# Optimization experiments

Hardware: AMD Instinct MI355X
Metric: run time of the kernel (lower is better)

Reference implementation:

```python
import jax, jax.numpy as jnp
import numpy as np

DIM = 192
NUM_HEADS = 6
WS = (2, 8, 8)          # (wd, wh, ww)
SHIFT = (1, 4, 4)
B, D, H, W = 2, 4, 128, 128
N_WIN_TOK = WS[0] * WS[1] * WS[2]   # 128
NW = (D // WS[0]) * (H // WS[1]) * (W // WS[2])  # 512 windows per sample


def _rel_pos_index(ws):
    d, h, w = ws
    coords = np.stack(np.meshgrid(np.arange(d), np.arange(h), np.arange(w), indexing='ij'))
    cf = coords.reshape(3, -1)
    rel = (cf[:, :, None] - cf[:, None, :]).transpose(1, 2, 0).astype(np.int64)
    rel[:, :, 0] += d - 1
    rel[:, :, 1] += h - 1
    rel[:, :, 2] += w - 1
    rel[:, :, 0] *= (2 * h - 1) * (2 * w - 1)
    rel[:, :, 1] *= 2 * w - 1
    return rel.sum(-1)  # (N, N)

REL_IDX = _rel_pos_index(WS)


def _sine_pos(HW, num_pos_feats, temperature=10000.0):
    # matches get_sine_position_encoding(normalize=True)
    scale = 2 * np.pi
    eps = 1e-6
    ones = np.ones((1, HW[0], HW[1]), np.float32)
    y = ones.cumsum(1)
    x = ones.cumsum(2)
    y = y / (y[:, -1:, :] + eps) * scale
    x = x / (x[:, :, -1:] + eps) * scale
    i = np.arange(num_pos_feats, dtype=np.float32)
    dim_t = temperature ** (2.0 * np.floor(i / 2) / num_pos_feats)
    px = x[:, :, :, None] / dim_t
    py = y[:, :, :, None] / dim_t
    px = np.stack((np.sin(px[..., 0::2]), np.cos(px[..., 1::2])), axis=4).reshape(1, HW[0], HW[1], -1)
    py = np.stack((np.sin(py[..., 0::2]), np.cos(py[..., 1::2])), axis=4).reshape(1, HW[0], HW[1], -1)
    pos = np.concatenate((py, px), axis=3)  # (1, H, W, 2*npf)
    return pos.reshape(1, HW[0] * HW[1], -1)

POS_BIAS = _sine_pos((WS[1], WS[2]), DIM // 2)  # (1, 64, DIM)


def _ln(x, w, b):
    mu = x.mean(-1, keepdims=True)
    var = x.var(-1, keepdims=True)
    return (x - mu) / jnp.sqrt(var + 1e-5) * w + b


def _qkv(x, w, b):
    B_, N, C = x.shape
    y = (x @ w.T + b).reshape(B_, N, 3, NUM_HEADS, C // NUM_HEADS).transpose(2, 0, 3, 1, 4)
    return y[0], y[1], y[2]  # each (B_, h, N, hd)


def _attn(q, k, v, mask, rpb=None):
    # q,k,v: (B_, h, N, hd); mask: (nW, N, N) or None; rpb: (h, N, N) or None
    scale = q.shape[-1] ** -0.5
    a = jnp.einsum('bhnd,bhmd->bhnm', q * scale, k)
    if rpb is not None:
        a = a + rpb[None]
    if mask is not None:
        B_, h, N, _ = a.shape
        nW = mask.shape[0]
        a = (a.reshape(B_ // nW, nW, h, N, N) + mask[None, :, None]).reshape(B_, h, N, N)
    a = jax.nn.softmax(a, axis=-1)
    out = jnp.einsum('bhnm,bhmd->bhnd', a, v)
    B_, h, N, hd = out.shape
    return out.transpose(0, 2, 1, 3).reshape(B_, N, h * hd)


def setup_inputs() -> dict:
    key = jax.random.key(0)
    ks = jax.random.split(key, 8)
    C = DIM
    hid = int(C * 2.0)
    f = lambda k, shp: jax.random.normal(k, shp, jnp.float32) * 0.02
    tbl = (2 * WS[0] - 1) * (2 * WS[1] - 1) * (2 * WS[2] - 1)
    return {
        'x': jax.random.normal(ks[0], (B, D, H, W, C), jnp.float32),
        'mask_matrix': jnp.zeros((NW, N_WIN_TOK, N_WIN_TOK), jnp.float32),
        'norm1_w': jnp.ones((C,), jnp.float32), 'norm1_b': jnp.zeros((C,), jnp.float32),
        'qkv_self_w': f(ks[1], (3 * C, C)), 'qkv_self_b': jnp.zeros((3 * C,), jnp.float32),
        'qkv_mut_w': f(ks[2], (3 * C, C)), 'qkv_mut_b': jnp.zeros((3 * C,), jnp.float32),
        'rpb_table': f(ks[3], (tbl, NUM_HEADS)),
        'proj_w': f(ks[4], (C, 2 * C)), 'proj_b': jnp.zeros((C,), jnp.float32),
        'norm2_w': jnp.ones((C,), jnp.float32), 'norm2_b': jnp.zeros((C,), jnp.float32),
        'fc11_w': f(ks[5], (hid, C)), 'fc11_b': jnp.zeros((hid,), jnp.float32),
        'fc12_w': f(ks[6], (hid, C)), 'fc12_b': jnp.zeros((hid,), jnp.float32),
        'fc2_w': f(ks[7], (C, hid)), 'fc2_b': jnp.zeros((C,), jnp.float32),
    }


def reference(x, mask_matrix, norm1_w, norm1_b, qkv_self_w, qkv_self_b,
              qkv_mut_w, qkv_mut_b, rpb_table, proj_w, proj_b,
              norm2_w, norm2_b, fc11_w, fc11_b, fc12_w, fc12_b, fc2_w, fc2_b):
    Bb, Dd, Hh, Ww_, C = x.shape
    wd, wh, ww = WS
    N = wd * wh * ww
    Nh = N // 2

    # ---- part1: windowed mutual+self attention with cyclic shift ----
    h1 = _ln(x, norm1_w, norm1_b)
    sh = jnp.roll(h1, (-SHIFT[0], -SHIFT[1], -SHIFT[2]), axis=(1, 2, 3))
    # window_partition -> (B*nW, N, C)
    xw = sh.reshape(Bb, Dd // wd, wd, Hh // wh, wh, Ww_ // ww, ww, C)
    xw = xw.transpose(0, 1, 3, 5, 2, 4, 6, 7).reshape(-1, N, C)

    # self-attention with relative position bias
    q, k, v = _qkv(xw, qkv_self_w, qkv_self_b)
    rpb = rpb_table[REL_IDX.reshape(-1)].reshape(N, N, NUM_HEADS).transpose(2, 0, 1)
    x_self = _attn(q, k, v, mask_matrix[:, :N, :N], rpb)  # (B_, N, C)

    # mutual attention (no relative bias), sine positional bias added to input
    pos = jnp.tile(jnp.asarray(POS_BIAS, x.dtype), (1, 2, 1))  # (1, N, C)
    q, k, v = _qkv(xw + pos, qkv_mut_w, qkv_mut_b)
    q1, q2 = q[:, :, :Nh], q[:, :, Nh:]
    k1, k2 = k[:, :, :Nh], k[:, :, Nh:]
    v1, v2 = v[:, :, :Nh], v[:, :, Nh:]
    m2 = mask_matrix[:, :Nh, :Nh]
    x1 = _attn(q2, k1, v1, m2)  # frame2 queries attend frame1
    x2 = _attn(q1, k2, v2, m2)
    x_out = jnp.concatenate([jnp.concatenate([x1, x2], axis=1), x_self], axis=2)  # (B_, N, 2C)
    xp = x_out @ proj_w.T + proj_b  # (B_, N, C)

    # window_reverse + roll back
    rev = xp.reshape(Bb, Dd // wd, Hh // wh, Ww_ // ww, wd, wh, ww, C)
    rev = rev.transpose(0, 1, 4, 2, 5, 3, 6, 7).reshape(Bb, Dd, Hh, Ww_, C)
    rev = jnp.roll(rev, SHIFT, axis=(1, 2, 3))
    x = x + rev

    # ---- part2: GEGLU MLP ----
    h2 = _ln(x, norm2_w, norm2_b)
    mlp = (jax.nn.gelu(h2 @ fc11_w.T + fc11_b, approximate=False) * (h2 @ fc12_w.T + fc12_b)) @ fc2_w.T + fc2_b
    return x + mlp
```

## Files before the change

kernel.cpp:

```cpp
#include <hip/hip_runtime.h>
#include <hip/hip_bf16.h>

typedef __hip_bfloat16 bf16;
typedef __attribute__((ext_vector_type(8))) short short8;
typedef __attribute__((ext_vector_type(4))) float f32x4;

#define NTOKENS 131072
#define MFMA __builtin_amdgcn_mfma_f32_16x16x32_bf16

static constexpr size_t A_OFF    = 0;
static constexpr size_t Q_OFF    = A_OFF   + (size_t)NTOKENS*192*2;
static constexpr size_t O_OFF    = Q_OFF   + (size_t)NTOKENS*576*2;
static constexpr size_t POS_OFF  = O_OFF   + (size_t)NTOKENS*384*2;
static constexpr size_t PB_OFF   = POS_OFF + (size_t)128*192*4;
static constexpr size_t RPBF_OFF = PB_OFF  + (size_t)128*576*4;
static constexpr size_t MSKF_OFF = RPBF_OFF+ (size_t)6*128*128*2;
static constexpr size_t WB_OFF   = MSKF_OFF+ (size_t)512*128*128*2;
static constexpr size_t WQS_E = 0, WQM_E = 110592, WPR_E = 221184,
                        W11_E = 294912, W12_E = 368640, W2_E = 442368, WTOT = 516096;

__device__ __forceinline__ float u2f(unsigned int ubits) {
    union { unsigned int i; float f; } c; c.i = ubits << 16; return c.f;
}
__device__ __forceinline__ unsigned pkbf(float a, float b) {
    unsigned ua = (unsigned)__bfloat16_as_ushort(__float2bfloat16(a));
    unsigned ub = (unsigned)__bfloat16_as_ushort(__float2bfloat16(b));
    return ua | (ub << 16);
}
__device__ __forceinline__ short8 u4s8(uint4 v) { union { uint4 u; short8 s; } c; c.u = v; return c.s; }

__device__ __forceinline__ void gl16(const bf16* g, void* l) {
    __builtin_amdgcn_global_load_lds(
        (const __attribute__((address_space(1))) void*)g,
        (__attribute__((address_space(3))) void*)l, 16, 0, 0);
}

__global__ __launch_bounds__(256) void cvtw_kernel(
    const float* __restrict__ a, const float* __restrict__ b, const float* __restrict__ c,
    const float* __restrict__ d, const float* __restrict__ e, const float* __restrict__ f,
    bf16* __restrict__ out) {
    int i = blockIdx.x * 256 + threadIdx.x;
    const float* src; int off;
    if      (i < (int)WQM_E) { src = a; off = (int)WQS_E; }
    else if (i < (int)WPR_E) { src = b; off = (int)WQM_E; }
    else if (i < (int)W11_E) { src = c; off = (int)WPR_E; }
    else if (i < (int)W12_E) { src = d; off = (int)W11_E; }
    else if (i < (int)W2_E)  { src = e; off = (int)W12_E; }
    else if (i < (int)WTOT)  { src = f; off = (int)W2_E; }
    else return;
    out[i] = __float2bfloat16(src[i - off]);
}

__global__ __launch_bounds__(256) void pos_kernel(float* __restrict__ pos) {
    int idx = blockIdx.x * 256 + threadIdx.x;
    if (idx >= 128 * 192) return;
    int t = idx / 192, c = idx - t * 192;
    int s = t & 63;
    int hh = s >> 3, ww = s & 7;
    const float twopi = 6.2831853071795864f;
    float coord = (c < 96) ? (float)(hh + 1) : (float)(ww + 1);
    coord = coord / (8.0f + 1e-6f) * twopi;
    int f = (c < 96) ? c : c - 96;
    float dimt = powf(10000.0f, (float)(2 * (f >> 1)) / 96.0f);
    float v = coord / dimt;
    pos[idx] = (f & 1) ? cosf(v) : sinf(v);
}

__global__ __launch_bounds__(256) void pbias_kernel(const float* __restrict__ pos,
                                                    const bf16* __restrict__ Wm,
                                                    const float* __restrict__ bqm,
                                                    float* __restrict__ PB) {
    int idx = blockIdx.x * 256 + threadIdx.x;
    if (idx >= 128 * 576) return;
    int t = idx / 576, n = idx - t * 576;
    const float* pp = pos + t * 192;
    const bf16* wp = Wm + (size_t)n * 192;
    float acc = bqm[n];
    for (int k = 0; k < 192; ++k) acc += pp[k] * __bfloat162float(wp[k]);
    PB[idx] = acc;
}

__global__ __launch_bounds__(256) void rpbF_kernel(const float* __restrict__ tbl,
                                                   bf16* __restrict__ rpbF) {
    int idx = blockIdx.x * 256 + threadIdx.x;
    if (idx >= 6 * 32 * 128 * 4) return;
    int jr = idx & 3;
    int i = (idx >> 2) & 127;
    int jq = (idx >> 9) & 31;
    int h = idx >> 14;
    int j = jq * 4 + jr;
    int di = i >> 6, hi = (i >> 3) & 7, wi = i & 7;
    int dj = j >> 6, hj = (j >> 3) & 7, wj = j & 7;
    int t = (di - dj + 1) * 225 + (hi - hj + 7) * 15 + (wi - wj + 7);
    rpbF[idx] = __float2bfloat16(tbl[t * 6 + h]);
}

__global__ __launch_bounds__(256) void mskF_kernel(const float* __restrict__ mask,
                                                   bf16* __restrict__ mskF) {
    int idx = blockIdx.x * 256 + threadIdx.x;
    int widx = idx >> 12;
    int rem = idx & 4095;
    int i = rem >> 5, jq = rem & 31;
    float4 v = *reinterpret_cast<const float4*>(mask + ((size_t)widx << 14) + i * 128 + jq * 4);
    uint2 o;
    o.x = pkbf(v.x, v.y);
    o.y = pkbf(v.z, v.w);
    *reinterpret_cast<uint2*>(mskF + ((size_t)widx << 14) + (jq * 128 + i) * 4) = o;
}

template <int PART>
__global__ __launch_bounds__(256) void ln_kernel(const float* __restrict__ xin,
                                                 const float* __restrict__ w,
                                                 const float* __restrict__ b,
                                                 bf16* __restrict__ out) {
    int tok = blockIdx.x * 4 + (threadIdx.x >> 6);
    int lane = threadIdx.x & 63;
    const float* xp = xin + (size_t)tok * 192;
    float x0 = xp[lane], x1 = xp[lane + 64], x2 = xp[lane + 128];
    float s = x0 + x1 + x2;
    float ss = x0 * x0 + x1 * x1 + x2 * x2;
    for (int off = 32; off; off >>= 1) {
        s += __shfl_xor(s, off);
        ss += __shfl_xor(ss, off);
    }
    float mean = s * (1.0f / 192.0f);
    float var = ss * (1.0f / 192.0f) - mean * mean;
    float rstd = rsqrtf(var + 1e-5f);
    size_t obase;
    if (PART) {
        int bb = tok >> 16;
        int rem = tok & 65535;
        int d = rem >> 14;
        int hw = rem & 16383;
        int hh = hw >> 7, w2 = hw & 127;
        int sd = (d + 3) & 3;
        int sh = (hh + 124) & 127;
        int sw = (w2 + 124) & 127;
        int win = ((bb * 2 + (sd >> 1)) * 16 + (sh >> 3)) * 16 + (sw >> 3);
        int t = ((sd & 1) << 6) | ((sh & 7) << 3) | (sw & 7);
        obase = ((size_t)win * 128 + t) * 192;
    } else {
        obase = (size_t)tok * 192;
    }
    out[obase + lane]       = __float2bfloat16((x0 - mean) * rstd * w[lane] + b[lane]);
    out[obase + lane + 64]  = __float2bfloat16((x1 - mean) * rstd * w[lane + 64] + b[lane + 64]);
    out[obase + lane + 128] = __float2bfloat16((x2 - mean) * rstd * w[lane + 128] + b[lane + 128]);
}

template <int MODE, int BIAS>
__global__ __launch_bounds__(256) void mgemm(
    const bf16* __restrict__ Ab, int K, int nb,
    const bf16* __restrict__ W1, const float* __restrict__ B1,
    const bf16* __restrict__ W2, const float* __restrict__ B2,
    const float* __restrict__ resid,
    void* __restrict__ outp) {
    constexpr bool DUAL = (MODE == 3);
    __shared__ __align__(16) unsigned char AsB[2][16384];

    int total = gridDim.x;
    int bid = blockIdx.x;
    int lin = (bid & 7) * (total >> 3) + (bid >> 3);
    int mb = lin / nb, nbk = lin - mb * nb;
    int m0 = mb << 7, n0 = nbk << 6;
    int tid = threadIdx.x;
    int w = tid >> 6, l = tid & 63;
    int wr = w >> 1, wc = w & 1;
    int lr = l & 15, lg = l >> 4;

    f32x4 acc[4][2] = {};
    f32x4 acc2[4][2] = {};

    auto stage = [&](int buf, int kc) {
        int k0 = kc << 6;
#pragma unroll
        for (int it = 0; it < 4; ++it) {
            int idx = it * 256 + tid;
            int row = idx >> 3, gs = idx & 7;
            int gsrc = gs ^ (row & 7);
            gl16(Ab + (size_t)(m0 + row) * K + k0 + gsrc * 8, &AsB[buf][idx * 16]);
        }
    };

    const bf16* wbase  = W1 + (size_t)(n0 + wc * 32 + lr) * K + lg * 8;
    const bf16* wbase2 = DUAL ? (W2 + (size_t)(n0 + wc * 32 + lr) * K + lg * 8) : wbase;

    uint4 wcur[2][2], wnxt[2][2];
    uint4 wcur2[2][2], wnxt2[2][2];

    int nK = K >> 6;
    stage(0, 0);
#pragma unroll
    for (int cb = 0; cb < 2; ++cb)
#pragma unroll
        for (int ks = 0; ks < 2; ++ks) {
            wcur[cb][ks] = *reinterpret_cast<const uint4*>(wbase + (size_t)cb * 16 * K + ks * 32);
            if constexpr (DUAL)
                wcur2[cb][ks] = *reinterpret_cast<const uint4*>(wbase2 + (size_t)cb * 16 * K + ks * 32);
        }
    __syncthreads();
    for (int kc = 0; kc < nK; ++kc) {
        int cur = kc & 1;
        if (kc + 1 < nK) {
            stage(cur ^ 1, kc + 1);
            int ko = (kc + 1) * 64;
#pragma unroll
            for (int cb = 0; cb < 2; ++cb)
#pragma unroll
                for (int ks = 0; ks < 2; ++ks) {
                    wnxt[cb][ks] = *reinterpret_cast<const uint4*>(
                        wbase + (size_t)cb * 16 * K + ko + ks * 32);
                    if constexpr (DUAL)
                        wnxt2[cb][ks] = *reinterpret_cast<const uint4*>(
                            wbase2 + (size_t)cb * 16 * K + ko + ks * 32);
                }
        }
        const unsigned char* as = AsB[cur];
#pragma unroll
        for (int ks = 0; ks < 2; ++ks) {
            short8 af[4];
#pragma unroll
            for (int rb = 0; rb < 4; ++rb) {
                int row = wr * 64 + rb * 16 + lr;
                af[rb] = *reinterpret_cast<const short8*>(
                    &as[(unsigned)((row * 128 + ks * 64 + lg * 16) ^ ((row & 7) << 4))]);
            }
#pragma unroll
            for (int rb = 0; rb < 4; ++rb)
#pragma unroll
                for (int cb = 0; cb < 2; ++cb) {
                    acc[rb][cb] = MFMA(af[rb], u4s8(wcur[cb][ks]), acc[rb][cb], 0, 0, 0);
                    if constexpr (DUAL)
                        acc2[rb][cb] = MFMA(af[rb], u4s8(wcur2[cb][ks]), acc2[rb][cb], 0, 0, 0);
                }
        }
        __syncthreads();
        if (kc + 1 < nK) {
#pragma unroll
            for (int cb = 0; cb < 2; ++cb)
#pragma unroll
                for (int ks = 0; ks < 2; ++ks) {
                    wcur[cb][ks] = wnxt[cb][ks];
                    if constexpr (DUAL) wcur2[cb][ks] = wnxt2[cb][ks];
                }
        }
    }

    if (MODE == 0 || MODE == 3) {
        bf16* eb = (bf16*)AsB[0];
#pragma unroll
        for (int rb = 0; rb < 4; ++rb)
#pragma unroll
            for (int r = 0; r < 4; ++r) {
                int ml = wr * 64 + rb * 16 + lg * 4 + r;
#pragma unroll
                for (int cb = 0; cb < 2; ++cb) {
                    int cl = wc * 32 + cb * 16 + lr;
                    int n = n0 + cl;
                    if (MODE == 0) {
                        float bias_v = BIAS ? resid[(ml & 127) * 576 + n] : B1[n];
                        eb[ml * 64 + cl] = __float2bfloat16(acc[rb][cb][r] + bias_v);
                    } else {
                        float u = acc[rb][cb][r] + B1[n];
                        float v2 = acc2[rb][cb][r] + B2[n];
                        float t = u * (0.7978845608028654f + 0.0356774081363001f * u * u);
                        float g = u * v2 / (1.0f + __expf(-2.0f * t));
                        eb[ml * 64 + cl] = __float2bfloat16(g);
                    }
                }
            }
        __syncthreads();
        bf16* Og = (bf16*)outp;
        const int ostr = (MODE == 0) ? 576 : 384;
#pragma unroll
        for (int it = 0; it < 4; ++it) {
            int idx = it * 256 + tid;
            int row = idx >> 3, g = idx & 7;
            uint4 v = *reinterpret_cast<const uint4*>(&eb[row * 64 + g * 8]);
            *reinterpret_cast<uint4*>(Og + (size_t)(m0 + row) * ostr + n0 + g * 8) = v;
        }
    } else {
#pragma unroll
        for (int rb = 0; rb < 4; ++rb) {
#pragma unroll
            for (int r = 0; r < 4; ++r) {
                int m = m0 + wr * 64 + rb * 16 + lg * 4 + r;
                if (MODE == 2) {
                    int win = m >> 7, t = m & 127;
                    int bb = win >> 9, rem = win & 511;
                    int sd = ((rem >> 8) << 1) | (t >> 6);
                    int sh = (((rem >> 4) & 15) << 3) | ((t >> 3) & 7);
                    int sw = ((rem & 15) << 3) | (t & 7);
                    int dq = (sd + 1) & 3;
                    int hq = (sh + 4) & 127;
                    int wq = (sw + 4) & 127;
                    size_t gb = ((((size_t)bb * 4 + dq) * 128 + hq) * 128 + wq) * 192;
                    float* Rr = (float*)outp;
#pragma unroll
                    for (int cb = 0; cb < 2; ++cb) {
                        int n = n0 + wc * 32 + cb * 16 + lr;
                        Rr[gb + n] = resid[gb + n] + acc[rb][cb][r] + B1[n];
                    }
                } else {
                    float* Og = (float*)outp;
#pragma unroll
                    for (int cb = 0; cb < 2; ++cb) {
                        int n = n0 + wc * 32 + cb * 16 + lr;
                        Og[(size_t)m * 192 + n] =
                            resid[(size_t)m * 192 + n] + acc[rb][cb][r] + B1[n];
                    }
                }
            }
        }
    }
}

__global__ __launch_bounds__(256) void attn_self(
    const bf16* __restrict__ Qb, const bf16* __restrict__ rpbF,
    const bf16* __restrict__ mskF, bf16* __restrict__ Ob) {
    __shared__ __align__(16) bf16 VtB[4096];
    __shared__ __align__(16) bf16 EpiB[4][1280];
    int bid = blockIdx.x;
    int lin = (bid & 7) * 768 + (bid >> 3);
    int widx = lin / 12, sub = lin - widx * 12;
    int h = sub % 6, b2 = sub / 6;
    int win = b2 * 512 + widx;
    int tid = threadIdx.x, w = tid >> 6, l = tid & 63;
    int lr = l & 15, lg = l >> 4;
    const float qscale = 0.17677669529663689f;
    size_t qbase = (size_t)win * 128 * 576 + h * 32;

#pragma unroll
    for (int it = 0; it < 16; ++it) {
        int idx = it * 256 + tid;
        int d = idx & 31, j = idx >> 5;
        bf16 v = Qb[qbase + (size_t)j * 576 + 384 + d];
        VtB[(d * 256 + (((j >> 3) ^ (d & 7)) << 4) + (j & 7) * 2) >> 1] = v;
    }

    uint4 kf[8], qf[2];
#pragma unroll
    for (int jb = 0; jb < 8; ++jb)
        kf[jb] = *reinterpret_cast<const uint4*>(Qb + qbase + (size_t)(jb * 16 + lr) * 576 + 192 + lg * 8);
    int i0 = w * 32;
#pragma unroll
    for (int ib = 0; ib < 2; ++ib)
        qf[ib] = *reinterpret_cast<const uint4*>(Qb + qbase + (size_t)(i0 + ib * 16 + lr) * 576 + lg * 8);
    f32x4 s[8][2] = {};
#pragma unroll
    for (int jb = 0; jb < 8; ++jb)
#pragma unroll
        for (int ib = 0; ib < 2; ++ib)
            s[jb][ib] = MFMA(u4s8(kf[jb]), u4s8(qf[ib]), s[jb][ib], 0, 0, 0);

    const bf16* rpF = rpbF + (size_t)h * 16384;
    const bf16* mpF = mskF + (size_t)widx * 16384;
#pragma unroll
    for (int jb = 0; jb < 8; ++jb) {
        int jq0 = jb * 4 + lg;
#pragma unroll
        for (int ib = 0; ib < 2; ++ib) {
            int il = i0 + ib * 16 + lr;
            uint2 rv = *reinterpret_cast<const uint2*>(rpF + (jq0 * 128 + il) * 4);
            uint2 mv = *reinterpret_cast<const uint2*>(mpF + (jq0 * 128 + il) * 4);
            s[jb][ib][0] = fmaf(s[jb][ib][0], qscale, u2f(rv.x & 0xffffu) + u2f(mv.x & 0xffffu));
            s[jb][ib][1] = fmaf(s[jb][ib][1], qscale, u2f(rv.x >> 16) + u2f(mv.x >> 16));
            s[jb][ib][2] = fmaf(s[jb][ib][2], qscale, u2f(rv.y & 0xffffu) + u2f(mv.y & 0xffffu));
            s[jb][ib][3] = fmaf(s[jb][ib][3], qscale, u2f(rv.y >> 16) + u2f(mv.y >> 16));
        }
    }

    float rs[2];
    unsigned w0[2][8], w1[2][8];
#pragma unroll
    for (int ib = 0; ib < 2; ++ib) {
        float mx = -1e30f;
#pragma unroll
        for (int jb = 0; jb < 8; ++jb)
#pragma unroll
            for (int r = 0; r < 4; ++r) mx = fmaxf(mx, s[jb][ib][r]);
        mx = fmaxf(mx, __shfl_xor(mx, 16));
        mx = fmaxf(mx, __shfl_xor(mx, 32));
        float sum = 0.0f;
#pragma unroll
        for (int jb = 0; jb < 8; ++jb)
#pragma unroll
            for (int r = 0; r < 4; ++r) {
                float e = __expf(s[jb][ib][r] - mx);
                s[jb][ib][r] = e;
                sum += e;
            }
        sum += __shfl_xor(sum, 16);
        sum += __shfl_xor(sum, 32);
        rs[ib] = 1.0f / sum;
#pragma unroll
        for (int jb = 0; jb < 8; ++jb) {
            w0[ib][jb] = pkbf(s[jb][ib][0], s[jb][ib][1]);
            w1[ib][jb] = pkbf(s[jb][ib][2], s[jb][ib][3]);
        }
    }
    __syncthreads();

    f32x4 o[2][2] = {};
    int srcA = lr + 16 * (2 * (lg & 1));
    int srcB = srcA + 16;
    bool hi = ((lg >> 1) & 1) != 0;
#pragma unroll
    for (int ks = 0; ks < 4; ++ks) {
        short8 vt[2];
#pragma unroll
        for (int db = 0; db < 2; ++db) {
            int d = db * 16 + lr;
            vt[db] = *reinterpret_cast<const short8*>(
                &VtB[(d * 256 + (((ks * 4 + lg) ^ (d & 7)) << 4)) >> 1]);
        }
#pragma unroll
        for (int ib = 0; ib < 2; ++ib) {
            unsigned xa0 = (unsigned)__shfl((int)w0[ib][2 * ks], srcA, 64);
            unsigned xa1 = (unsigned)__shfl((int)w0[ib][2 * ks + 1], srcA, 64);
            unsigned xb0 = (unsigned)__shfl((int)w1[ib][2 * ks], srcA, 64);
            unsigned xb1 = (unsigned)__shfl((int)w1[ib][2 * ks + 1], srcA, 64);
            unsigned xc0 = (unsigned)__shfl((int)w0[ib][2 * ks], srcB, 64);
            unsigned xc1 = (unsigned)__shfl((int)w0[ib][2 * ks + 1], srcB, 64);
            unsigned xd0 = (unsigned)__shfl((int)w1[ib][2 * ks], srcB, 64);
            unsigned xd1 = (unsigned)__shfl((int)w1[ib][2 * ks + 1], srcB, 64);
            uint4 bfv;
            bfv.x = hi ? xa1 : xa0;
            bfv.y = hi ? xb1 : xb0;
            bfv.z = hi ? xc1 : xc0;
            bfv.w = hi ? xd1 : xd0;
            short8 pb = u4s8(bfv);
#pragma unroll
            for (int db = 0; db < 2; ++db) o[db][ib] = MFMA(vt[db], pb, o[db][ib], 0, 0, 0);
        }
    }

    bf16* eb = &EpiB[w][0];
#pragma unroll
    for (int db = 0; db < 2; ++db)
#pragma unroll
        for (int ib = 0; ib < 2; ++ib)
#pragma unroll
            for (int r = 0; r < 4; ++r) {
                int d = db * 16 + lg * 4 + r;
                int il = ib * 16 + lr;
                eb[il * 40 + d] = __float2bfloat16(o[db][ib][r] * rs[ib]);
            }
    int il2 = l >> 1, hf = l & 1;
    uint4 oa = *reinterpret_cast<const uint4*>(&eb[il2 * 40 + hf * 16]);
    uint4 ob2 = *reinterpret_cast<const uint4*>(&eb[il2 * 40 + hf * 16 + 8]);
    size_t gbase = ((size_t)win * 128 + i0 + il2) * 384 + 192 + h * 32 + hf * 16;
    *reinterpret_cast<uint4*>(Ob + gbase) = oa;
    *reinterpret_cast<uint4*>(Ob + gbase + 8) = ob2;
}

__global__ __launch_bounds__(256) void attn_mut(
    const bf16* __restrict__ Qb, const bf16* __restrict__ mskF, bf16* __restrict__ Ob) {
    __shared__ __align__(16) bf16 VtB[4096];
    __shared__ __align__(16) bf16 EpiB[4][1280];
    int bid = blockIdx.x;
    int lin = (bid & 7) * 768 + (bid >> 3);
    int widx = lin / 12, sub = lin - widx * 12;
    int h = sub % 6, b2 = sub / 6;
    int win = b2 * 512 + widx;
    int tid = threadIdx.x, w = tid >> 6, l = tid & 63;
    int lr = l & 15, lg = l >> 4;
    const float qscale = 0.17677669529663689f;
    size_t qbase = (size_t)win * 128 * 576 + h * 32;

#pragma unroll
    for (int it = 0; it < 16; ++it) {
        int idx = it * 256 + tid;
        int d = idx & 31, j = idx >> 5;
        bf16 v = Qb[qbase + (size_t)j * 576 + 384 + d];
        VtB[(d * 256 + (((j >> 3) ^ (d & 7)) << 4) + (j & 7) * 2) >> 1] = v;
    }

    int i0 = w * 32;
    int qoff = (w < 2) ? 64 : -64;
    int koff = (w < 2) ? 0 : 64;
    uint4 kf[4], qf[2];
#pragma unroll
    for (int jb = 0; jb < 4; ++jb)
        kf[jb] = *reinterpret_cast<const uint4*>(
            Qb + qbase + (size_t)(koff + jb * 16 + lr) * 576 + 192 + lg * 8);
#pragma unroll
    for (int ib = 0; ib < 2; ++ib)
        qf[ib] = *reinterpret_cast<const uint4*>(
            Qb + qbase + (size_t)(i0 + ib * 16 + lr + qoff) * 576 + lg * 8);
    f32x4 s[4][2] = {};
#pragma unroll
    for (int jb = 0; jb < 4; ++jb)
#pragma unroll
        for (int ib = 0; ib < 2; ++ib)
            s[jb][ib] = MFMA(u4s8(kf[jb]), u4s8(qf[ib]), s[jb][ib], 0, 0, 0);

    const bf16* mpF = mskF + (size_t)widx * 16384;
    int ibase = (i0 & 63);
#pragma unroll
    for (int jb = 0; jb < 4; ++jb) {
        int jq0 = jb * 4 + lg;
#pragma unroll
        for (int ib = 0; ib < 2; ++ib) {
            int il = ibase + ib * 16 + lr;
            uint2 mv = *reinterpret_cast<const uint2*>(mpF + (jq0 * 128 + il) * 4);
            s[jb][ib][0] = fmaf(s[jb][ib][0], qscale, u2f(mv.x & 0xffffu));
            s[jb][ib][1] = fmaf(s[jb][ib][1], qscale, u2f(mv.x >> 16));
            s[jb][ib][2] = fmaf(s[jb][ib][2], qscale, u2f(mv.y & 0xffffu));
            s[jb][ib][3] = fmaf(s[jb][ib][3], qscale, u2f(mv.y >> 16));
        }
    }

    float rs[2];
    unsigned w0[2][4], w1[2][4];
#pragma unroll
    for (int ib = 0; ib < 2; ++ib) {
        float mx = -1e30f;
#pragma unroll
        for (int jb = 0; jb < 4; ++jb)
#pragma unroll
            for (int r = 0; r < 4; ++r) mx = fmaxf(mx, s[jb][ib][r]);
        mx = fmaxf(mx, __shfl_xor(mx, 16));
        mx = fmaxf(mx, __shfl_xor(mx, 32));
        float sum = 0.0f;
#pragma unroll
        for (int jb = 0; jb < 4; ++jb)
#pragma unroll
            for (int r = 0; r < 4; ++r) {
                float e = __expf(s[jb][ib][r] - mx);
                s[jb][ib][r] = e;
                sum += e;
            }
        sum += __shfl_xor(sum, 16);
        sum += __shfl_xor(sum, 32);
        rs[ib] = 1.0f / sum;
#pragma unroll
        for (int jb = 0; jb < 4; ++jb) {
            w0[ib][jb] = pkbf(s[jb][ib][0], s[jb][ib][1]);
            w1[ib][jb] = pkbf(s[jb][ib][2], s[jb][ib][3]);
        }
    }
    __syncthreads();

    f32x4 o[2][2] = {};
    int srcA = lr + 16 * (2 * (lg & 1));
    int srcB = srcA + 16;
    bool hi = ((lg >> 1) & 1) != 0;
    int gb0 = koff >> 3;
#pragma unroll
    for (int ks = 0; ks < 2; ++ks) {
        short8 vt[2];
#pragma unroll
        for (int db = 0; db < 2; ++db) {
            int d = db * 16 + lr;
            vt[db] = *reinterpret_cast<const short8*>(
                &VtB[(d * 256 + (((gb0 + ks * 4 + lg) ^ (d & 7)) << 4)) >> 1]);
        }
#pragma unroll
        for (int ib = 0; ib < 2; ++ib) {
            unsigned xa0 = (unsigned)__shfl((int)w0[ib][2 * ks], srcA, 64);
            unsigned xa1 = (unsigned)__shfl((int)w0[ib][2 * ks + 1], srcA, 64);
            unsigned xb0 = (unsigned)__shfl((int)w1[ib][2 * ks], srcA, 64);
            unsigned xb1 = (unsigned)__shfl((int)w1[ib][2 * ks + 1], srcA, 64);
            unsigned xc0 = (unsigned)__shfl((int)w0[ib][2 * ks], srcB, 64);
            unsigned xc1 = (unsigned)__shfl((int)w0[ib][2 * ks + 1], srcB, 64);
            unsigned xd0 = (unsigned)__shfl((int)w1[ib][2 * ks], srcB, 64);
            unsigned xd1 = (unsigned)__shfl((int)w1[ib][2 * ks + 1], srcB, 64);
            uint4 bfv;
            bfv.x = hi ? xa1 : xa0;
            bfv.y = hi ? xb1 : xb0;
            bfv.z = hi ? xc1 : xc0;
            bfv.w = hi ? xd1 : xd0;
            short8 pb = u4s8(bfv);
#pragma unroll
            for (int db = 0; db < 2; ++db) o[db][ib] = MFMA(vt[db], pb, o[db][ib], 0, 0, 0);
        }
    }

    bf16* eb = &EpiB[w][0];
#pragma unroll
    for (int db = 0; db < 2; ++db)
#pragma unroll
        for (int ib = 0; ib < 2; ++ib)
#pragma unroll
            for (int r = 0; r < 4; ++r) {
                int d = db * 16 + lg * 4 + r;
                int il = ib * 16 + lr;
                eb[il * 40 + d] = __float2bfloat16(o[db][ib][r] * rs[ib]);
            }
    int il2 = l >> 1, hf = l & 1;
    uint4 oa = *reinterpret_cast<const uint4*>(&eb[il2 * 40 + hf * 16]);
    uint4 ob2 = *reinterpret_cast<const uint4*>(&eb[il2 * 40 + hf * 16 + 8]);
    size_t gbase = ((size_t)win * 128 + i0 + il2) * 384 + h * 32 + hf * 16;
    *reinterpret_cast<uint4*>(Ob + gbase) = oa;
    *reinterpret_cast<uint4*>(Ob + gbase + 8) = ob2;
}

extern "C" void kernel_launch(void* const* d_in, const int* in_sizes, int n_in,
                              void* d_out, int out_size, void* d_ws, size_t ws_size,
                              hipStream_t stream) {
    const float* x    = (const float*)d_in[0];
    const float* mask = (const float*)d_in[1];
    const float* n1w  = (const float*)d_in[2];
    const float* n1b  = (const float*)d_in[3];
    const float* wqs  = (const float*)d_in[4];
    const float* bqs  = (const float*)d_in[5];
    const float* wqm  = (const float*)d_in[6];
    const float* bqm  = (const float*)d_in[7];
    const float* rpbt = (const float*)d_in[8];
    const float* wproj= (const float*)d_in[9];
    const float* bproj= (const float*)d_in[10];
    const float* n2w  = (const float*)d_in[11];
    const float* n2b  = (const float*)d_in[12];
    const float* w11  = (const float*)d_in[13];
    const float* b11  = (const float*)d_in[14];
    const float* w12  = (const float*)d_in[15];
    const float* b12  = (const float*)d_in[16];
    const float* w2   = (const float*)d_in[17];
    const float* b2   = (const float*)d_in[18];

    char* ws = (char*)d_ws;
    bf16*  A    = (bf16*)(ws + A_OFF);
    bf16*  Q    = (bf16*)(ws + Q_OFF);
    bf16*  O    = (bf16*)(ws + O_OFF);
    float* pos  = (float*)(ws + POS_OFF);
    float* PB   = (float*)(ws + PB_OFF);
    bf16*  rpbF = (bf16*)(ws + RPBF_OFF);
    bf16*  mskF = (bf16*)(ws + MSKF_OFF);
    bf16*  WB   = (bf16*)(ws + WB_OFF);
    bf16*  Hb = A;
    bf16*  G  = Q;
    float* R  = (float*)d_out;
    float* out = (float*)d_out;

    cvtw_kernel<<<(WTOT + 255) / 256, 256, 0, stream>>>(wqs, wqm, wproj, w11, w12, w2, WB);
    pos_kernel<<<96, 256, 0, stream>>>(pos);
    pbias_kernel<<<288, 256, 0, stream>>>(pos, WB + WQM_E, bqm, PB);
    rpbF_kernel<<<384, 256, 0, stream>>>(rpbt, rpbF);
    mskF_kernel<<<8192, 256, 0, stream>>>(mask, mskF);
    ln_kernel<1><<<32768, 256, 0, stream>>>(x, n1w, n1b, A);
    mgemm<0, 0><<<9 * 1024, 256, 0, stream>>>(A, 192, 9, WB + WQS_E, bqs, nullptr, nullptr,
                                              nullptr, Q);
    attn_self<<<6144, 256, 0, stream>>>(Q, rpbF, mskF, O);
    mgemm<0, 1><<<9 * 1024, 256, 0, stream>>>(A, 192, 9, WB + WQM_E, nullptr, nullptr, nullptr,
                                              PB, Q);
    attn_mut<<<6144, 256, 0, stream>>>(Q, mskF, O);
    mgemm<2, 0><<<3 * 1024, 256, 0, stream>>>(O, 384, 3, WB + WPR_E, bproj, nullptr, nullptr,
                                              x, R);
    ln_kernel<0><<<32768, 256, 0, stream>>>(R, n2w, n2b, Hb);
    mgemm<3, 0><<<6 * 1024, 256, 0, stream>>>(Hb, 192, 6, WB + W11_E, b11, WB + W12_E, b12,
                                              nullptr, G);
    mgemm<4, 0><<<3 * 1024, 256, 0, stream>>>(G, 384, 3, WB + W2_E, b2, nullptr, nullptr,
                                              R, out);
}
```

Measured before the change: 633.2 us.

## Stage GEMM weights through LDS and fuse LayerNorm2 into projection GEMM epilogue

The weight fragments for all mgemm variants now come through double-buffered, swizzled LDS tiles loaded asynchronously, replacing per-lane global register prefetch. The projection GEMM (MODE 2) is widened to cover all 192 output columns per block. This lets its epilogue compute the residual add and the full LayerNorm2 in-block, removing the separate ln_kernel launch and its reread of R. In exchange the kernel uses more shared memory and gets per-kernel launch-bound occupancy hints. The fused epilogue also adds two __syncthreads per output row and runs a much smaller grid for MODE 2.

Result: faster. 577.3 us (-8.8%).

```diff
diff --git a/kernel.cpp b/kernel.cpp
--- a/kernel.cpp
+++ b/kernel.cpp
@@ -148,27 +148,37 @@
 }
 
 template <int MODE, int BIAS>
-__global__ __launch_bounds__(256) void mgemm(
+__global__ __launch_bounds__(256, (MODE == 2 || MODE == 3) ? 2 : 3) void mgemm(
     const bf16* __restrict__ Ab, int K, int nb,
     const bf16* __restrict__ W1, const float* __restrict__ B1,
     const bf16* __restrict__ W2, const float* __restrict__ B2,
     const float* __restrict__ resid,
-    void* __restrict__ outp) {
-    constexpr bool DUAL = (MODE == 3);
-    __shared__ __align__(16) unsigned char AsB[2][16384];
+    void* __restrict__ outp,
+    const float* __restrict__ lnw, const float* __restrict__ lnb,
+    void* __restrict__ outp2) {
+    constexpr bool DUAL   = (MODE == 3);
+    constexpr int  NCB    = (MODE == 2) ? 6 : 2;
+    constexpr int  WCOL   = (MODE == 2) ? 96 : 32;
+    constexpr int  WROWS  = (MODE == 2) ? 192 : 64;
+    constexpr int  WBYTES = WROWS * 128;
+    constexpr int  POOL   = 32768 + 2 * WBYTES + (DUAL ? 2 * WBYTES : 0);
+    __shared__ __align__(16) unsigned char pool[POOL];
+    unsigned char* AsB0  = pool;
+    unsigned char* WsB0  = pool + 32768;
+    unsigned char* Ws2B0 = pool + 32768 + 2 * WBYTES;
 
     int total = gridDim.x;
     int bid = blockIdx.x;
     int lin = (bid & 7) * (total >> 3) + (bid >> 3);
     int mb = lin / nb, nbk = lin - mb * nb;
-    int m0 = mb << 7, n0 = nbk << 6;
+    int m0 = mb << 7, n0 = nbk * WROWS;
     int tid = threadIdx.x;
     int w = tid >> 6, l = tid & 63;
     int wr = w >> 1, wc = w & 1;
     int lr = l & 15, lg = l >> 4;
 
-    f32x4 acc[4][2] = {};
-    f32x4 acc2[4][2] = {};
+    f32x4 acc[4][NCB] = {};
+    f32x4 acc2[DUAL ? 4 : 1][DUAL ? NCB : 1] = {};
 
     auto stage = [&](int buf, int kc) {
         int k0 = kc << 6;
@@ -177,47 +187,31 @@
             int idx = it * 256 + tid;
             int row = idx >> 3, gs = idx & 7;
             int gsrc = gs ^ (row & 7);
-            gl16(Ab + (size_t)(m0 + row) * K + k0 + gsrc * 8, &AsB[buf][idx * 16]);
+            gl16(Ab + (size_t)(m0 + row) * K + k0 + gsrc * 8, AsB0 + buf * 16384 + idx * 16);
+        }
+#pragma unroll
+        for (int it = 0; it < WROWS / 32; ++it) {
+            int idx = it * 256 + tid;
+            int row = idx >> 3, gs = idx & 7;
+            int gsrc = gs ^ (row & 7);
+            gl16(W1 + (size_t)(n0 + row) * K + k0 + gsrc * 8, WsB0 + buf * WBYTES + idx * 16);
+            if constexpr (DUAL)
+                gl16(W2 + (size_t)(n0 + row) * K + k0 + gsrc * 8, Ws2B0 + buf * WBYTES + idx * 16);
         }
     };
-
-    const bf16* wbase  = W1 + (size_t)(n0 + wc * 32 + lr) * K + lg * 8;
-    const bf16* wbase2 = DUAL ? (W2 + (size_t)(n0 + wc * 32 + lr) * K + lg * 8) : wbase;
-
-    uint4 wcur[2][2], wnxt[2][2];
-    uint4 wcur2[2][2], wnxt2[2][2];
 
     int nK = K >> 6;
     stage(0, 0);
-#pragma unroll
-    for (int cb = 0; cb < 2; ++cb)
-#pragma unroll
-        for (int ks = 0; ks < 2; ++ks) {
-            wcur[cb][ks] = *reinterpret_cast<const uint4*>(wbase + (size_t)cb * 16 * K + ks * 32);
-            if constexpr (DUAL)
-                wcur2[cb][ks] = *reinterpret_cast<const uint4*>(wbase2 + (size_t)cb * 16 * K + ks * 32);
-        }
     __syncthreads();
     for (int kc = 0; kc < nK; ++kc) {
         int cur = kc & 1;
-        if (kc + 1 < nK) {
-            stage(cur ^ 1, kc + 1);
-            int ko = (kc + 1) * 64;
-#pragma unroll
-            for (int cb = 0; cb < 2; ++cb)
-#pragma unroll
-                for (int ks = 0; ks < 2; ++ks) {
-                    wnxt[cb][ks] = *reinterpret_cast<const uint4*>(
-                        wbase + (size_t)cb * 16 * K + ko + ks * 32);
-                    if constexpr (DUAL)
-                        wnxt2[cb][ks] = *reinterpret_cast<const uint4*>(
-                            wbase2 + (size_t)cb * 16 * K + ko + ks * 32);
-                }
-        }
-        const unsigned char* as = AsB[cur];
+        if (kc + 1 < nK) stage(cur ^ 1, kc + 1);
+        const unsigned char* as  = AsB0 + cur * 16384;
+        const unsigned char* wsb = WsB0 + cur * WBYTES;
+        const unsigned char* ws2 = DUAL ? (Ws2B0 + cur * WBYTES) : wsb;
 #pragma unroll
         for (int ks = 0; ks < 2; ++ks) {
-            short8 af[4];
+            short8 af[4], wf[NCB], wf2[DUAL ? NCB : 1];
 #pragma unroll
             for (int rb = 0; rb < 4; ++rb) {
                 int row = wr * 64 + rb * 16 + lr;
@@ -225,35 +219,34 @@
                     &as[(unsigned)((row * 128 + ks * 64 + lg * 16) ^ ((row & 7) << 4))]);
             }
 #pragma unroll
+            for (int cb = 0; cb < NCB; ++cb) {
+                int row = wc * WCOL + cb * 16 + lr;
+                unsigned off = (unsigned)((row * 128 + ks * 64 + lg * 16) ^ ((row & 7) << 4));
+                wf[cb] = *reinterpret_cast<const short8*>(&wsb[off]);
+                if constexpr (DUAL)
+                    wf2[cb] = *reinterpret_cast<const short8*>(&ws2[off]);
+            }
+#pragma unroll
             for (int rb = 0; rb < 4; ++rb)
 #pragma unroll
-                for (int cb = 0; cb < 2; ++cb) {
-                    acc[rb][cb] = MFMA(af[rb], u4s8(wcur[cb][ks]), acc[rb][cb], 0, 0, 0);
+                for (int cb = 0; cb < NCB; ++cb) {
+                    acc[rb][cb] = MFMA(af[rb], wf[cb], acc[rb][cb], 0, 0, 0);
                     if constexpr (DUAL)
-                        acc2[rb][cb] = MFMA(af[rb], u4s8(wcur2[cb][ks]), acc2[rb][cb], 0, 0, 0);
+                        acc2[rb][cb] = MFMA(af[rb], wf2[cb], acc2[rb][cb], 0, 0, 0);
                 }
         }
         __syncthreads();
-        if (kc + 1 < nK) {
-#pragma unroll
-            for (int cb = 0; cb < 2; ++cb)
-#pragma unroll
-                for (int ks = 0; ks < 2; ++ks) {
-                    wcur[cb][ks] = wnxt[cb][ks];
-                    if constexpr (DUAL) wcur2[cb][ks] = wnxt2[cb][ks];
-                }
-        }
     }
 
     if (MODE == 0 || MODE == 3) {
-        bf16* eb = (bf16*)AsB[0];
+        bf16* eb = (bf16*)pool;
 #pragma unroll
         for (int rb = 0; rb < 4; ++rb)
 #pragma unroll
             for (int r = 0; r < 4; ++r) {
                 int ml = wr * 64 + rb * 16 + lg * 4 + r;
 #pragma unroll
-                for (int cb = 0; cb < 2; ++cb) {
+                for (int cb = 0; cb < NCB; ++cb) {
                     int cl = wc * 32 + cb * 16 + lr;
                     int n = n0 + cl;
                     if (MODE == 0) {
@@ -278,36 +271,72 @@
             uint4 v = *reinterpret_cast<const uint4*>(&eb[row * 64 + g * 8]);
             *reinterpret_cast<uint4*>(Og + (size_t)(m0 + row) * ostr + n0 + g * 8) = v;
         }
+    } else if (MODE == 2) {
+        float* lnS = (float*)pool;
+        float* lnQ = (float*)(pool + 1024);
+        float* Rr  = (float*)outp;
+        bf16*  Hg  = (bf16*)outp2;
+#pragma unroll
+        for (int rb = 0; rb < 4; ++rb) {
+#pragma unroll
+            for (int r = 0; r < 4; ++r) {
+                int ml = wr * 64 + rb * 16 + lg * 4 + r;
+                int m = m0 + ml;
+                int win = m >> 7, t = m & 127;
+                int bb = win >> 9, rem = win & 511;
+                int sd = ((rem >> 8) << 1) | (t >> 6);
+                int sh = (((rem >> 4) & 15) << 3) | ((t >> 3) & 7);
+                int sw = ((rem & 15) << 3) | (t & 7);
+                int dq = (sd + 1) & 3;
+                int hq = (sh + 4) & 127;
+                int wq = (sw + 4) & 127;
+                size_t gb = ((((size_t)bb * 4 + dq) * 128 + hq) * 128 + wq) * 192;
+                float vals[6];
+                float s = 0.0f, ss = 0.0f;
+#pragma unroll
+                for (int cb = 0; cb < 6; ++cb) {
+                    int n = wc * 96 + cb * 16 + lr;
+                    float v = resid[gb + n] + acc[rb][cb][r] + B1[n];
+                    Rr[gb + n] = v;
+                    vals[cb] = v;
+                    s += v;
+                    ss += v * v;
+                }
+#pragma unroll
+                for (int off = 1; off < 16; off <<= 1) {
+                    s += __shfl_xor(s, off);
+                    ss += __shfl_xor(ss, off);
+                }
+                if (lr == 0) {
+                    lnS[ml * 2 + wc] = s;
+                    lnQ[ml * 2 + wc] = ss;
+                }
+                __syncthreads();
+                float st = lnS[ml * 2] + lnS[ml * 2 + 1];
+                float qt = lnQ[ml * 2] + lnQ[ml * 2 + 1];
+                float mean = st * (1.0f / 192.0f);
+                float var = qt * (1.0f / 192.0f) - mean * mean;
+                float rstd = rsqrtf(var + 1e-5f);
+#pragma unroll
+                for (int cb = 0; cb < 6; ++cb) {
+                    int n = wc * 96 + cb * 16 + lr;
+                    Hg[gb + n] = __float2bfloat16((vals[cb] - mean) * rstd * lnw[n] + lnb[n]);
+                }
+                __syncthreads();
+            }
+        }
     } else {
 #pragma unroll
         for (int rb = 0; rb < 4; ++rb) {
 #pragma unroll
             for (int r = 0; r < 4; ++r) {
                 int m = m0 + wr * 64 + rb * 16 + lg * 4 + r;
-                if (MODE == 2) {
-                    int win = m >> 7, t = m & 127;
-                    int bb = win >> 9, rem = win & 511;
-                    int sd = ((rem >> 8) << 1) | (t >> 6);
-                    int sh = (((rem >> 4) & 15) << 3) | ((t >> 3) & 7);
-                    int sw = ((rem & 15) << 3) | (t & 7);
-                    int dq = (sd + 1) & 3;
-                    int hq = (sh + 4) & 127;
-                    int wq = (sw + 4) & 127;
-                    size_t gb = ((((size_t)bb * 4 + dq) * 128 + hq) * 128 + wq) * 192;
-                    float* Rr = (float*)outp;
-#pragma unroll
-                    for (int cb = 0; cb < 2; ++cb) {
-                        int n = n0 + wc * 32 + cb * 16 + lr;
-                        Rr[gb + n] = resid[gb + n] + acc[rb][cb][r] + B1[n];
-                    }
-                } else {
-                    float* Og = (float*)outp;
-#pragma unroll
-                    for (int cb = 0; cb < 2; ++cb) {
-                        int n = n0 + wc * 32 + cb * 16 + lr;
-                        Og[(size_t)m * 192 + n] =
-                            resid[(size_t)m * 192 + n] + acc[rb][cb][r] + B1[n];
-                    }
+                float* Og = (float*)outp;
+#pragma unroll
+                for (int cb = 0; cb < NCB; ++cb) {
+                    int n = n0 + wc * 32 + cb * 16 + lr;
+                    Og[(size_t)m * 192 + n] =
+                        resid[(size_t)m * 192 + n] + acc[rb][cb][r] + B1[n];
                 }
             }
         }
@@ -639,16 +668,15 @@
     mskF_kernel<<<8192, 256, 0, stream>>>(mask, mskF);
     ln_kernel<1><<<32768, 256, 0, stream>>>(x, n1w, n1b, A);
     mgemm<0, 0><<<9 * 1024, 256, 0, stream>>>(A, 192, 9, WB + WQS_E, bqs, nullptr, nullptr,
-                                              nullptr, Q);
+                                              nullptr, Q, nullptr, nullptr, nullptr);
     attn_self<<<6144, 256, 0, stream>>>(Q, rpbF, mskF, O);
     mgemm<0, 1><<<9 * 1024, 256, 0, stream>>>(A, 192, 9, WB + WQM_E, nullptr, nullptr, nullptr,
-                                              PB, Q);
+                                              PB, Q, nullptr, nullptr, nullptr);
     attn_mut<<<6144, 256, 0, stream>>>(Q, mskF, O);
-    mgemm<2, 0><<<3 * 1024, 256, 0, stream>>>(O, 384, 3, WB + WPR_E, bproj, nullptr, nullptr,
-                                              x, R);
-    ln_kernel<0><<<32768, 256, 0, stream>>>(R, n2w, n2b, Hb);
+    mgemm<2, 0><<<1024, 256, 0, stream>>>(O, 384, 1, WB + WPR_E, bproj, nullptr, nullptr,
+                                          x, R, n2w, n2b, Hb);
     mgemm<3, 0><<<6 * 1024, 256, 0, stream>>>(Hb, 192, 6, WB + W11_E, b11, WB + W12_E, b12,
-                                              nullptr, G);
+                                              nullptr, G, nullptr, nullptr, nullptr);
     mgemm<4, 0><<<3 * 1024, 256, 0, stream>>>(G, 384, 3, WB + W2_E, b2, nullptr, nullptr,
-                                              R, out);
-}
+                                              R, out, nullptr, nullptr, nullptr);
+}
```
